# Kernel tuning notes

Hardware: AMD Instinct MI355X
Metric: run time of the kernel (lower is better)

Reference implementation:

```python
import jax, jax.numpy as jnp
import numpy as np

NUM_GROUPS = 32
EPS = 1e-6


def group_norm(x, gamma, beta):
    b, c, h, w = x.shape
    xg = x.reshape(b, NUM_GROUPS, c // NUM_GROUPS, h, w)
    mean = xg.mean(axis=(2, 3, 4), keepdims=True)
    var = xg.var(axis=(2, 3, 4), keepdims=True)
    xn = ((xg - mean) * jax.lax.rsqrt(var + EPS)).reshape(b, c, h, w)
    return xn * gamma[None, :, None, None] + beta[None, :, None, None]


def conv1x1(x, W, b):
    # x: [b,c,h,w], W: [c_out, c_in]
    return jnp.einsum('oi,bihw->bohw', W, x) + b[None, :, None, None]


def setup_inputs() -> dict:
    key = jax.random.key(0)
    ks = jax.random.split(key, 6)
    B, C, H, W = 4, 256, 64, 64
    s = 1.0 / np.sqrt(C)
    return {
        'x': jax.random.normal(ks[0], (B, C, H, W), jnp.float32),
        'gamma': jnp.ones((C,), jnp.float32),
        'beta': jnp.zeros((C,), jnp.float32),
        'Wq': jax.random.normal(ks[1], (C, C), jnp.float32) * s,
        'bq': jnp.zeros((C,), jnp.float32),
        'Wk': jax.random.normal(ks[2], (C, C), jnp.float32) * s,
        'bk': jnp.zeros((C,), jnp.float32),
        'Wv': jax.random.normal(ks[3], (C, C), jnp.float32) * s,
        'bv': jnp.zeros((C,), jnp.float32),
        'Wo': jax.random.normal(ks[4], (C, C), jnp.float32) * s,
        'bo': jnp.zeros((C,), jnp.float32),
    }


def reference(x, gamma, beta, Wq, bq, Wk, bk, Wv, bv, Wo, bo):
    attn_num = 1
    b, c, h, w = x.shape
    hn = group_norm(x, gamma, beta)
    q = conv1x1(hn, Wq, bq)
    k = conv1x1(hn, Wk, bk)
    v = conv1x1(hn, Wv, bv)
    ch = c // attn_num
    n = h * w
    q = q.reshape(b * attn_num, ch, n)
    k = k.reshape(b * attn_num, ch, n)
    v = v.reshape(b * attn_num, ch, n)
    # scores[g, i, j] = sum_c q[g,c,i] * k[g,c,j]; NOTE: scaled by full c, as in source
    scores = jnp.einsum('gci,gcj->gij', q, k) * (float(c) ** -0.5)
    attn = jax.nn.softmax(scores, axis=2)
    # h_[g,c,i] = sum_j v[g,c,j] * attn[g,i,j]
    out = jnp.einsum('gcj,gij->gci', v, attn).reshape(b, c, h, w)
    out = conv1x1(out, Wo, bo)
    return x + out
```

## Files before the change

### kernel.cpp

```cpp
#include <hip/hip_runtime.h>

typedef __attribute__((ext_vector_type(4))) float f32x4;
typedef __attribute__((ext_vector_type(8))) __bf16 bf16x8;

__device__ __forceinline__ unsigned short f2bf(float f) {
  unsigned int u = __float_as_uint(f);
  u += 0x7FFFu + ((u >> 16) & 1u);
  return (unsigned short)(u >> 16);
}
__device__ __forceinline__ float bf2f(unsigned short u) {
  return __uint_as_float(((unsigned int)u) << 16);
}
__device__ __forceinline__ float ex2(float x) {
  return __builtin_amdgcn_exp2f(x);
}

__device__ __forceinline__ void gload16(const void* g, void* l) {
  __builtin_amdgcn_global_load_lds(
      (const __attribute__((address_space(1))) void*)g,
      (__attribute__((address_space(3))) void*)l, 16, 0, 0);
}

#define QSCALE 0.09016844005555897f

__global__ __launch_bounds__(256)
void prep_weights(const float* __restrict__ wq, const float* __restrict__ wk,
                  const float* __restrict__ wv, const float* __restrict__ wo,
                  unsigned short* __restrict__ out) {
  int i = blockIdx.x * 256 + threadIdx.x;
  const float* src = (i < 65536) ? wq : (i < 131072) ? wk : (i < 196608) ? wv : wo;
  out[i] = f2bf(src[i & 65535]);
}

__global__ __launch_bounds__(1024)
void groupnorm_kernel(const float* __restrict__ x, const float* __restrict__ gamma,
                      const float* __restrict__ beta, unsigned short* __restrict__ hnT) {
  const int blk = blockIdx.x;
  const int b = blk >> 5, g = blk & 31;
  const int N = 4096;
  const float* xb = x + ((size_t)b * 256 + (size_t)g * 8) * N;
  const int tid = threadIdx.x;

  float s = 0.f, ss = 0.f;
  for (int c = 0; c < 8; ++c) {
    const float* xc = xb + (size_t)c * N;
    for (int i = tid; i < N; i += 1024) { float v = xc[i]; s += v; ss += v * v; }
  }
  __shared__ float rs[16], rss[16];
  for (int m = 1; m <= 32; m <<= 1) { s += __shfl_xor(s, m); ss += __shfl_xor(ss, m); }
  const int lane = tid & 63, wid = tid >> 6;
  if (lane == 0) { rs[wid] = s; rss[wid] = ss; }
  __syncthreads();
  s = 0.f; ss = 0.f;
  #pragma unroll
  for (int i = 0; i < 16; ++i) { s += rs[i]; ss += rss[i]; }
  const float mean = s * (1.f / 32768.f);
  const float var  = ss * (1.f / 32768.f) - mean * mean;
  const float rstd = rsqrtf(var + 1e-6f);

  float gk[8], bk2[8];
  #pragma unroll
  for (int c = 0; c < 8; ++c) {
    float ga = gamma[g * 8 + c] * rstd;
    gk[c]  = ga;
    bk2[c] = beta[g * 8 + c] - mean * ga;
  }
  unsigned short* outp = hnT + (size_t)b * 256 * N + g * 8;
  for (int i = tid; i < N; i += 1024) {
    union { unsigned short u[8]; uint4 v; } pk;
    #pragma unroll
    for (int c = 0; c < 8; ++c) pk.u[c] = f2bf(xb[(size_t)c * N + i] * gk[c] + bk2[c]);
    *reinterpret_cast<uint4*>(outp + (size_t)i * 256) = pk.v;
  }
}

__global__ __launch_bounds__(256, 2)
void qkv_fused(const unsigned short* __restrict__ WB,
               const unsigned short* __restrict__ hnT,
               const float* __restrict__ bq, const float* __restrict__ bk,
               const float* __restrict__ bv,
               unsigned short* __restrict__ Qt, unsigned short* __restrict__ Kt,
               unsigned short* __restrict__ Vp) {
  __shared__ alignas(1024) unsigned char lds[32768];
  const int tid = threadIdx.x, lane = tid & 63, w = tid >> 6;
  const int hig = lane >> 4, l15 = lane & 15;
  const int z = blockIdx.y, nt = blockIdx.x;
  const int n0 = nt * 32;
  const size_t zoff = (size_t)z * 1048576;
  const unsigned short* hnB = hnT + zoff + (size_t)n0 * 256;

  #pragma unroll
  for (int p = 0; p < 4; ++p) {
    const int idx = p * 256 + tid;
    const int r = idx >> 5, sl = idx & 31;
    gload16(hnB + (size_t)r * 256 + ((sl ^ (r & 7)) << 3), lds + idx * 16);
  }

  const int qs = (lane & 3) ^ ((lane >> 3) & 3);
  const int ar = tid >> 2, asq = tid & 3;
  auto stageA = [&](int d, int s) {
    const unsigned short* base = WB + (s >> 3) * 32768 + (s & 7) * 32 + qs * 8;
    unsigned char* dst = lds + 16384 + d * 8192;
    gload16(base + (size_t)ar * 256,        dst + ar * 64 + asq * 16);
    gload16(base + (size_t)(ar + 64) * 256, dst + (ar + 64) * 64 + asq * 16);
  };

  const int aslot = hig ^ ((l15 >> 1) & 3);
  f32x4 acc[2][2] = {};

  stageA(0, 0);
  __syncthreads();

  for (int s = 0; s < 48; ++s) {
    const int d = s & 1;
    if (s + 1 < 48) stageA(d ^ 1, s + 1);
    const int kt = s & 7;
    bf16x8 af[2];
    #pragma unroll
    for (int mf = 0; mf < 2; ++mf)
      af[mf] = *reinterpret_cast<const bf16x8*>(
          lds + 16384 + d * 8192 + (w * 32 + mf * 16 + l15) * 64 + aslot * 16);
    #pragma unroll
    for (int nf = 0; nf < 2; ++nf) {
      const int rb = nf * 16 + l15;
      bf16x8 bfr = *reinterpret_cast<const bf16x8*>(
          lds + rb * 512 + (((kt * 4 + hig) ^ (rb & 7)) << 4));
      acc[0][nf] = __builtin_amdgcn_mfma_f32_16x16x32_bf16(af[0], bfr, acc[0][nf], 0, 0, 0);
      acc[1][nf] = __builtin_amdgcn_mfma_f32_16x16x32_bf16(af[1], bfr, acc[1][nf], 0, 0, 0);
    }
    if (kt == 7) {
      const int sel = s >> 3, wsel = sel >> 1, mh = sel & 1;
      #pragma unroll
      for (int mf = 0; mf < 2; ++mf) {
        const int gm0 = mh * 128 + w * 32 + mf * 16 + 4 * hig;
        #pragma unroll
        for (int nf = 0; nf < 2; ++nf) {
          const int n = n0 + nf * 16 + l15;
          if (wsel == 0) {
            ushort4 pk;
            pk.x = f2bf((acc[mf][nf][0] + bq[gm0])     * QSCALE);
            pk.y = f2bf((acc[mf][nf][1] + bq[gm0 + 1]) * QSCALE);
            pk.z = f2bf((acc[mf][nf][2] + bq[gm0 + 2]) * QSCALE);
            pk.w = f2bf((acc[mf][nf][3] + bq[gm0 + 3]) * QSCALE);
            *reinterpret_cast<ushort4*>(Qt + zoff + (size_t)n * 256 + gm0) = pk;
          } else if (wsel == 1) {
            ushort4 pk;
            pk.x = f2bf(acc[mf][nf][0] + bk[gm0]);
            pk.y = f2bf(acc[mf][nf][1] + bk[gm0 + 1]);
            pk.z = f2bf(acc[mf][nf][2] + bk[gm0 + 2]);
            pk.w = f2bf(acc[mf][nf][3] + bk[gm0 + 3]);
            *reinterpret_cast<ushort4*>(Kt + zoff + (size_t)n * 256 + gm0) = pk;
          } else {
            #pragma unroll
            for (int e = 0; e < 4; ++e)
              Vp[zoff + (size_t)(gm0 + e) * 4096 + n] = f2bf(acc[mf][nf][e] + bv[gm0 + e]);
          }
          acc[mf][nf] = f32x4{0.f, 0.f, 0.f, 0.f};
        }
      }
    }
    __syncthreads();
  }
}

__global__ __launch_bounds__(256, 2)
void flash_attn(const unsigned short* __restrict__ Qt,
                const unsigned short* __restrict__ Kt,
                const unsigned short* __restrict__ Vp,
                unsigned short* __restrict__ Opart, float* __restrict__ lpart) {
  __shared__ alignas(1024) unsigned char lds[81920];
  const int tid = threadIdx.x, lane = tid & 63, w = tid >> 6;
  const int hig = lane >> 4, l15 = lane & 15;
  const int bid = blockIdx.x;
  const int xcd = bid & 7, k = bid >> 3;
  const int combo = xcd * 2 + (k >> 5);
  const int jh = combo & 3, z = combo >> 2, qtb = k & 31;
  const size_t zoff = (size_t)z * 1048576;
  const unsigned short* Qz = Qt + zoff;
  const unsigned short* Kz = Kt + zoff;
  const unsigned short* Vz = Vp + zoff;
  const int q0 = qtb * 128 + w * 32;
  const int jb0 = jh * 1024;

  bf16x8 qfr[2][8];
  #pragma unroll
  for (int qf = 0; qf < 2; ++qf)
    #pragma unroll
    for (int ks = 0; ks < 8; ++ks)
      qfr[qf][ks] = *reinterpret_cast<const bf16x8*>(
          Qz + (size_t)(q0 + qf * 16 + l15) * 256 + ks * 32 + hig * 8);

  unsigned char* Pw = lds + 65536 + w * 4096;

  const unsigned short* pK[4];
  const unsigned short* pV[4];
  #pragma unroll
  for (int g = 0; g < 4; ++g) {
    const int jr = w * 8 + g * 2 + (lane >> 5);
    pK[g] = Kz + (size_t)(jb0 + jr) * 256 + (((lane & 31) ^ (jr & 7)) << 3);
    const int rloc = lane >> 3;
    const int sraw = (lane & 7) ^ rloc;
    const int cV = 2 * (w * 32 + g * 8 + rloc) + (sraw >> 2);
    pV[g] = Vz + (size_t)cV * 4096 + jb0 + (sraw & 3) * 8;
  }

  auto stage = [&](int d, int t) {
    unsigned char* Kd = lds + d * 16384 + w * 4096;
    unsigned char* Vd = lds + 32768 + d * 16384 + w * 4096;
    #pragma unroll
    for (int g = 0; g < 4; ++g) gload16(pK[g] + (size_t)t * 8192, Kd + g * 1024);
    #pragma unroll
    for (int g = 0; g < 4; ++g) gload16(pV[g] + (size_t)t * 32, Vd + g * 1024);
  };

  f32x4 o0[16] = {}, o1[16] = {};
  float l0 = 0.f, l1 = 0.f;

  stage(0, 0);
  for (int t = 0; t < 32; ++t) {
    asm volatile("s_waitcnt vmcnt(0)" ::: "memory");
    __builtin_amdgcn_s_barrier();
    __builtin_amdgcn_sched_barrier(0);
    const int cur = t & 1;
    if (t + 1 < 32) stage(cur ^ 1, t + 1);

    const unsigned char* Kb = lds + cur * 16384;
    const unsigned char* Vb = lds + 32768 + cur * 16384;

    f32x4 sA[2][2] = {};
    __builtin_amdgcn_s_setprio(1);
    #pragma unroll
    for (int ks = 0; ks < 8; ++ks) {
      #pragma unroll
      for (int jf = 0; jf < 2; ++jf) {
        const int jl = jf * 16 + l15;
        bf16x8 kf = *reinterpret_cast<const bf16x8*>(
            Kb + jl * 512 + (((4 * ks + hig) ^ (jl & 7)) << 4));
        sA[jf][0] = __builtin_amdgcn_mfma_f32_16x16x32_bf16(kf, qfr[0][ks], sA[jf][0], 0, 0, 0);
        sA[jf][1] = __builtin_amdgcn_mfma_f32_16x16x32_bf16(kf, qfr[1][ks], sA[jf][1], 0, 0, 0);
      }
    }
    __builtin_amdgcn_s_setprio(0);

    #pragma unroll
    for (int jf = 0; jf < 2; ++jf) {
      const int so = (((2 * jf + (hig >> 1)) ^ (l15 & 7)) << 4) + ((hig & 1) << 3);
      {
        float p0 = ex2(sA[jf][0][0]), p1 = ex2(sA[jf][0][1]);
        float p2 = ex2(sA[jf][0][2]), p3 = ex2(sA[jf][0][3]);
        l0 += (p0 + p1) + (p2 + p3);
        union { __bf16 b[4]; uint2 u; } pk;
        pk.b[0] = (__bf16)p0; pk.b[1] = (__bf16)p1;
        pk.b[2] = (__bf16)p2; pk.b[3] = (__bf16)p3;
        *reinterpret_cast<uint2*>(Pw + l15 * 128 + so) = pk.u;
      }
      {
        float p0 = ex2(sA[jf][1][0]), p1 = ex2(sA[jf][1][1]);
        float p2 = ex2(sA[jf][1][2]), p3 = ex2(sA[jf][1][3]);
        l1 += (p0 + p1) + (p2 + p3);
        union { __bf16 b[4]; uint2 u; } pk;
        pk.b[0] = (__bf16)p0; pk.b[1] = (__bf16)p1;
        pk.b[2] = (__bf16)p2; pk.b[3] = (__bf16)p3;
        *reinterpret_cast<uint2*>(Pw + (16 + l15) * 128 + so) = pk.u;
      }
    }

    const int pso = (hig ^ (l15 & 7)) << 4;
    bf16x8 pa0 = *reinterpret_cast<const bf16x8*>(Pw + l15 * 128 + pso);
    bf16x8 pa1 = *reinterpret_cast<const bf16x8*>(Pw + (16 + l15) * 128 + pso);
    const int vslot = ((l15 & 1) * 4 + hig) ^ (l15 >> 1);
    __builtin_amdgcn_s_setprio(1);
    #pragma unroll
    for (int nf = 0; nf < 16; ++nf) {
      bf16x8 vb = *reinterpret_cast<const bf16x8*>(
          Vb + (8 * nf + (l15 >> 1)) * 128 + (vslot << 4));
      o0[nf] = __builtin_amdgcn_mfma_f32_16x16x32_bf16(pa0, vb, o0[nf], 0, 0, 0);
      o1[nf] = __builtin_amdgcn_mfma_f32_16x16x32_bf16(pa1, vb, o1[nf], 0, 0, 0);
    }
    __builtin_amdgcn_s_setprio(0);
  }

  l0 += __shfl_xor(l0, 16); l0 += __shfl_xor(l0, 32);
  l1 += __shfl_xor(l1, 16); l1 += __shfl_xor(l1, 32);

  unsigned short* Ob = Opart + ((size_t)(jh * 4 + z) * 4096 + q0) * 256;
  #pragma unroll
  for (int qf = 0; qf < 2; ++qf)
    #pragma unroll
    for (int nf = 0; nf < 16; ++nf)
      #pragma unroll
      for (int e = 0; e < 4; ++e) {
        const int row = qf * 16 + 4 * hig + e;
        Ob[(size_t)row * 256 + nf * 16 + l15] = f2bf((qf == 0) ? o0[nf][e] : o1[nf][e]);
      }
  if (hig == 0) {
    const size_t mb = (size_t)(jh * 4 + z) * 4096 + q0;
    lpart[mb + l15] = l0;  lpart[mb + 16 + l15] = l1;
  }
}

__global__ __launch_bounds__(256)
void flash_merge(const unsigned short* __restrict__ Opart,
                 const float* __restrict__ lpart, unsigned short* __restrict__ Ht) {
  const int t = threadIdx.x;
  const int r = blockIdx.x * 4 + (t >> 6);
  const int c = (t & 63) * 4;
  const int z = r >> 12, n = r & 4095;
  float lsum = 0.f;
  #pragma unroll
  for (int h = 0; h < 4; ++h) lsum += lpart[(h * 4 + z) * 4096 + n];
  const float inv = 1.f / lsum;
  float acc[4] = {};
  #pragma unroll
  for (int h = 0; h < 4; ++h) {
    ushort4 v = *reinterpret_cast<const ushort4*>(
        Opart + ((size_t)((h * 4 + z) * 4096 + n)) * 256 + c);
    acc[0] += bf2f(v.x); acc[1] += bf2f(v.y);
    acc[2] += bf2f(v.z); acc[3] += bf2f(v.w);
  }
  ushort4 pk;
  pk.x = f2bf(acc[0] * inv); pk.y = f2bf(acc[1] * inv);
  pk.z = f2bf(acc[2] * inv); pk.w = f2bf(acc[3] * inv);
  *reinterpret_cast<ushort4*>(Ht + (size_t)r * 256 + c) = pk;
}

__global__ __launch_bounds__(256)
void gemm_out(const unsigned short* __restrict__ A,
              const unsigned short* __restrict__ B, long bStrideZ,
              float* __restrict__ Out, long oStrideZ,
              const float* __restrict__ bias,
              const float* __restrict__ resid, long rStrideZ,
              int M, int N, int K) {
  __shared__ alignas(1024) unsigned char lds[32768];
  const int tid  = threadIdx.x;
  const int lane = tid & 63;
  const int hi   = lane >> 4;
  const int l15  = lane & 15;
  const int wid  = tid >> 6;
  const int wm = wid >> 1, wn = wid & 1;
  const int z  = blockIdx.z;
  const int m0 = blockIdx.y * 128;
  const int n0 = blockIdx.x * 128;
  const unsigned short* Az = A;
  const unsigned short* Bz = B + (size_t)z * bStrideZ;

  const int c0 = wid * 2, c1 = wid * 2 + 1;
  const int rr = lane >> 2;
  const int qs = (lane & 3) ^ ((lane >> 3) & 3);
  const unsigned short* pa0 = Az + (size_t)(m0 + c0 * 16 + rr) * K + qs * 8;
  const unsigned short* pa1 = Az + (size_t)(m0 + c1 * 16 + rr) * K + qs * 8;
  const unsigned short* pb0 = Bz + (size_t)(n0 + c0 * 16 + rr) * K + qs * 8;
  const unsigned short* pb1 = Bz + (size_t)(n0 + c1 * 16 + rr) * K + qs * 8;
  unsigned char* lA0 = lds + c0 * 1024;
  unsigned char* lA1 = lds + c1 * 1024;
  unsigned char* lB0 = lds + 8192 + c0 * 1024;
  unsigned char* lB1 = lds + 8192 + c1 * 1024;

  const int slot = hi ^ ((l15 >> 1) & 3);
  int roffA[4], roffB[4];
  #pragma unroll
  for (int t = 0; t < 4; ++t) {
    roffA[t] = (wm * 64 + t * 16 + l15) * 64 + slot * 16;
    roffB[t] = 8192 + (wn * 64 + t * 16 + l15) * 64 + slot * 16;
  }

  f32x4 acc[4][4] = {};

  const int nk = K >> 5;
  gload16(pa0, lA0); gload16(pa1, lA1);
  gload16(pb0, lB0); gload16(pb1, lB1);
  __syncthreads();

  int cur = 0;
  for (int kt = 0; kt < nk; ++kt) {
    if (kt + 1 < nk) {
      const size_t ko = (size_t)(kt + 1) * 32;
      const int bo = (cur ^ 1) * 16384;
      gload16(pa0 + ko, lA0 + bo); gload16(pa1 + ko, lA1 + bo);
      gload16(pb0 + ko, lB0 + bo); gload16(pb1 + ko, lB1 + bo);
    }
    const unsigned char* base = lds + cur * 16384;
    bf16x8 af[4], bfr[4];
    #pragma unroll
    for (int t = 0; t < 4; ++t) {
      af[t]  = *reinterpret_cast<const bf16x8*>(base + roffA[t]);
      bfr[t] = *reinterpret_cast<const bf16x8*>(base + roffB[t]);
    }
    #pragma unroll
    for (int mt = 0; mt < 4; ++mt)
      #pragma unroll
      for (int nt = 0; nt < 4; ++nt)
        acc[mt][nt] = __builtin_amdgcn_mfma_f32_16x16x32_bf16(af[mt], bfr[nt], acc[mt][nt], 0, 0, 0);
    __syncthreads();
    cur ^= 1;
  }

  const int gmb = m0 + wm * 64;
  const int gnb = n0 + wn * 64;
  float* O = Out + (size_t)z * oStrideZ;
  const float* R = resid + (size_t)z * rStrideZ;
  #pragma unroll
  for (int mt = 0; mt < 4; ++mt) {
    const int gm0 = gmb + mt * 16 + 4 * hi;
    #pragma unroll
    for (int nt = 0; nt < 4; ++nt) {
      const int gn = gnb + nt * 16 + l15;
      #pragma unroll
      for (int e = 0; e < 4; ++e) {
        size_t idx = (size_t)(gm0 + e) * N + gn;
        O[idx] = acc[mt][nt][e] + bias[gm0 + e] + R[idx];
      }
    }
  }
}

__global__ void ws_too_small(float* out, float v) {
  if (threadIdx.x == 0 && blockIdx.x == 0) out[0] = v;
}

extern "C" void kernel_launch(void* const* d_in, const int* in_sizes, int n_in,
                              void* d_out, int out_size, void* d_ws, size_t ws_size,
                              hipStream_t stream) {
  const float* x     = (const float*)d_in[0];
  const float* gamma = (const float*)d_in[1];
  const float* beta  = (const float*)d_in[2];
  const float* Wq    = (const float*)d_in[3];
  const float* bq    = (const float*)d_in[4];
  const float* Wk    = (const float*)d_in[5];
  const float* bk    = (const float*)d_in[6];
  const float* Wv    = (const float*)d_in[7];
  const float* bv    = (const float*)d_in[8];
  const float* Wo    = (const float*)d_in[9];
  const float* bo    = (const float*)d_in[10];
  float* out = (float*)d_out;

  unsigned char* ws = (unsigned char*)d_ws;
  unsigned short* WB    = (unsigned short*)(ws);
  unsigned short* hnT   = (unsigned short*)(ws + 524288);
  float*          lpart = (float*)(ws + 524288);
  unsigned short* Qt    = (unsigned short*)(ws + 8912896);
  unsigned short* Kt    = (unsigned short*)(ws + 17301504);
  unsigned short* V     = (unsigned short*)(ws + 25690112);
  unsigned short* Ht    = (unsigned short*)(ws + 34078720);
  unsigned short* Opart = (unsigned short*)(ws + 42467328);

  if (ws_size < 76283904) {
    hipMemsetAsync(d_out, 0, (size_t)out_size * 4, stream);
    ws_too_small<<<1, 64, 0, stream>>>(out, (float)ws_size);
    return;
  }

  prep_weights<<<1024, 256, 0, stream>>>(Wq, Wk, Wv, Wo, WB);
  groupnorm_kernel<<<128, 1024, 0, stream>>>(x, gamma, beta, hnT);

  qkv_fused<<<dim3(128, 4), 256, 0, stream>>>(WB, hnT, bq, bk, bv, Qt, Kt, V);

  flash_attn<<<512, 256, 0, stream>>>(Qt, Kt, V, Opart, lpart);
  flash_merge<<<4096, 256, 0, stream>>>(Opart, lpart, Ht);

  gemm_out<<<dim3(32, 2, 4), 256, 0, stream>>>(
      WB + 196608, Ht, 1048576, out, 1048576, bo, x, 1048576, 256, 4096, 256);
}
```

Baseline: 145.3 us.

## Split groupnorm across twice as many blocks using cooperative grid sync

Replaces the 128-block groupnorm with a 256-block cooperative kernel. Each block handles half of a (batch, group) slice, keeps its values in registers, writes partial sums, synchronizes the whole grid, then normalizes and writes the bf16 transposed output. The aim is to use more of the GPU's CUs for this memory-bound step and avoid re-reading x. In exchange it depends on cooperative launch and pays for a grid-wide barrier, and it falls back to the old kernel if the launch fails.

```diff
diff --git a/kernel.cpp b/kernel.cpp
--- a/kernel.cpp
+++ b/kernel.cpp
@@ -1,4 +1,7 @@
 #include <hip/hip_runtime.h>
+#include <hip/hip_cooperative_groups.h>
+
+namespace cg = cooperative_groups;
 
 typedef __attribute__((ext_vector_type(4))) float f32x4;
 typedef __attribute__((ext_vector_type(8))) __bf16 bf16x8;
@@ -30,6 +33,61 @@
   int i = blockIdx.x * 256 + threadIdx.x;
   const float* src = (i < 65536) ? wq : (i < 131072) ? wk : (i < 196608) ? wv : wo;
   out[i] = f2bf(src[i & 65535]);
+}
+
+__global__ __launch_bounds__(512)
+void groupnorm_coop(const float* __restrict__ x, const float* __restrict__ gamma,
+                    const float* __restrict__ beta, unsigned short* __restrict__ hnT,
+                    float2* __restrict__ part) {
+  const int blk = blockIdx.x;
+  const int h = blk & 1, bg = blk >> 1;
+  const int b = bg >> 5, g = bg & 31;
+  const int tid = threadIdx.x;
+  const float* xb = x + ((size_t)b * 256 + (size_t)g * 8) * 4096 + h * 2048;
+
+  float v[8][4];
+  float s = 0.f, ss = 0.f;
+  #pragma unroll
+  for (int c = 0; c < 8; ++c)
+    #pragma unroll
+    for (int s2 = 0; s2 < 4; ++s2) {
+      float val = xb[c * 4096 + s2 * 512 + tid];
+      v[c][s2] = val; s += val; ss += val * val;
+    }
+  __shared__ float rs[8], rss[8];
+  for (int m = 1; m <= 32; m <<= 1) { s += __shfl_xor(s, m); ss += __shfl_xor(ss, m); }
+  const int lane = tid & 63, wid = tid >> 6;
+  if (lane == 0) { rs[wid] = s; rss[wid] = ss; }
+  __syncthreads();
+  if (tid == 0) {
+    float a = 0.f, b2 = 0.f;
+    #pragma unroll
+    for (int i = 0; i < 8; ++i) { a += rs[i]; b2 += rss[i]; }
+    part[blk] = make_float2(a, b2);
+  }
+  cg::this_grid().sync();
+  const int base = blk & ~1;
+  const float2 p0 = part[base], p1 = part[base + 1];
+  const float mean = (p0.x + p1.x) * (1.f / 32768.f);
+  const float var  = (p0.y + p1.y) * (1.f / 32768.f) - mean * mean;
+  const float rstd = rsqrtf(var + 1e-6f);
+
+  float gk[8], bk2[8];
+  #pragma unroll
+  for (int c = 0; c < 8; ++c) {
+    float ga = gamma[g * 8 + c] * rstd;
+    gk[c]  = ga;
+    bk2[c] = beta[g * 8 + c] - mean * ga;
+  }
+  unsigned short* outp = hnT + (size_t)b * 4096 * 256 + g * 8;
+  #pragma unroll
+  for (int s2 = 0; s2 < 4; ++s2) {
+    const int n = h * 2048 + s2 * 512 + tid;
+    union { unsigned short u[8]; uint4 q; } pk;
+    #pragma unroll
+    for (int c = 0; c < 8; ++c) pk.u[c] = f2bf(v[c][s2] * gk[c] + bk2[c]);
+    *reinterpret_cast<uint4*>(outp + (size_t)n * 256) = pk.q;
+  }
 }
 
 __global__ __launch_bounds__(1024)
@@ -443,6 +501,7 @@
   unsigned short* V     = (unsigned short*)(ws + 25690112);
   unsigned short* Ht    = (unsigned short*)(ws + 34078720);
   unsigned short* Opart = (unsigned short*)(ws + 42467328);
+  float2*         gnpart = (float2*)(ws + 76021760);
 
   if (ws_size < 76283904) {
     hipMemsetAsync(d_out, 0, (size_t)out_size * 4, stream);
@@ -451,7 +510,15 @@
   }
 
   prep_weights<<<1024, 256, 0, stream>>>(Wq, Wk, Wv, Wo, WB);
-  groupnorm_kernel<<<128, 1024, 0, stream>>>(x, gamma, beta, hnT);
+
+  {
+    void* gnargs[] = {(void*)&x, (void*)&gamma, (void*)&beta, (void*)&hnT, (void*)&gnpart};
+    hipError_t ce = hipLaunchCooperativeKernel((const void*)groupnorm_coop,
+                                               dim3(256), dim3(512), gnargs, 0, stream);
+    if (ce != hipSuccess) {
+      groupnorm_kernel<<<128, 1024, 0, stream>>>(x, gamma, beta, hnT);
+    }
+  }
 
   qkv_fused<<<dim3(128, 4), 256, 0, stream>>>(WB, hnT, bq, bk, bv, Qt, Kt, V);
 
```

Result: slower. 169.9 us (+17.0%).

## Split group-norm across two blocks per group and keep inputs in registers

Applied to the files above, without the earlier changes.

The group-norm kernel now launches 256 blocks of 512 threads, so each group is handled by two blocks, and the grid covers more compute units than the old 128-block launch. Each block keeps its half of the group in registers and reuses those values for the normalized output instead of reading x a second time. To get full-group statistics, each block still reads the other half, so total reads stay roughly the same but are spread over twice as many blocks. Holding 32 values per thread raises register pressure.

```diff
diff --git a/kernel.cpp b/kernel.cpp
--- a/kernel.cpp
+++ b/kernel.cpp
@@ -32,28 +32,41 @@
   out[i] = f2bf(src[i & 65535]);
 }
 
-__global__ __launch_bounds__(1024)
-void groupnorm_kernel(const float* __restrict__ x, const float* __restrict__ gamma,
-                      const float* __restrict__ beta, unsigned short* __restrict__ hnT) {
+__global__ __launch_bounds__(512)
+void groupnorm_split(const float* __restrict__ x, const float* __restrict__ gamma,
+                     const float* __restrict__ beta, unsigned short* __restrict__ hnT) {
   const int blk = blockIdx.x;
-  const int b = blk >> 5, g = blk & 31;
-  const int N = 4096;
-  const float* xb = x + ((size_t)b * 256 + (size_t)g * 8) * N;
+  const int h = blk & 1, bg = blk >> 1;
+  const int b = bg >> 5, g = bg & 31;
   const int tid = threadIdx.x;
-
+  const float* xg = x + ((size_t)b * 256 + (size_t)g * 8) * 4096;
+  const float* xo = xg + h * 2048;
+  const float* xr = xg + (h ^ 1) * 2048;
+
+  float v[8][4];
   float s = 0.f, ss = 0.f;
-  for (int c = 0; c < 8; ++c) {
-    const float* xc = xb + (size_t)c * N;
-    for (int i = tid; i < N; i += 1024) { float v = xc[i]; s += v; ss += v * v; }
-  }
-  __shared__ float rs[16], rss[16];
+  #pragma unroll
+  for (int c = 0; c < 8; ++c)
+    #pragma unroll
+    for (int s2 = 0; s2 < 4; ++s2) {
+      float val = xo[c * 4096 + s2 * 512 + tid];
+      v[c][s2] = val; s += val; ss += val * val;
+    }
+  #pragma unroll
+  for (int c = 0; c < 8; ++c)
+    #pragma unroll
+    for (int s2 = 0; s2 < 4; ++s2) {
+      float val = xr[c * 4096 + s2 * 512 + tid];
+      s += val; ss += val * val;
+    }
+  __shared__ float rs[8], rss[8];
   for (int m = 1; m <= 32; m <<= 1) { s += __shfl_xor(s, m); ss += __shfl_xor(ss, m); }
   const int lane = tid & 63, wid = tid >> 6;
   if (lane == 0) { rs[wid] = s; rss[wid] = ss; }
   __syncthreads();
   s = 0.f; ss = 0.f;
   #pragma unroll
-  for (int i = 0; i < 16; ++i) { s += rs[i]; ss += rss[i]; }
+  for (int i = 0; i < 8; ++i) { s += rs[i]; ss += rss[i]; }
   const float mean = s * (1.f / 32768.f);
   const float var  = ss * (1.f / 32768.f) - mean * mean;
   const float rstd = rsqrtf(var + 1e-6f);
@@ -65,12 +78,14 @@
     gk[c]  = ga;
     bk2[c] = beta[g * 8 + c] - mean * ga;
   }
-  unsigned short* outp = hnT + (size_t)b * 256 * N + g * 8;
-  for (int i = tid; i < N; i += 1024) {
-    union { unsigned short u[8]; uint4 v; } pk;
-    #pragma unroll
-    for (int c = 0; c < 8; ++c) pk.u[c] = f2bf(xb[(size_t)c * N + i] * gk[c] + bk2[c]);
-    *reinterpret_cast<uint4*>(outp + (size_t)i * 256) = pk.v;
+  unsigned short* outp = hnT + (size_t)b * 4096 * 256 + g * 8;
+  #pragma unroll
+  for (int s2 = 0; s2 < 4; ++s2) {
+    const int n = h * 2048 + s2 * 512 + tid;
+    union { unsigned short u[8]; uint4 q; } pk;
+    #pragma unroll
+    for (int c = 0; c < 8; ++c) pk.u[c] = f2bf(v[c][s2] * gk[c] + bk2[c]);
+    *reinterpret_cast<uint4*>(outp + (size_t)n * 256) = pk.q;
   }
 }
 
@@ -451,7 +466,7 @@
   }
 
   prep_weights<<<1024, 256, 0, stream>>>(Wq, Wk, Wv, Wo, WB);
-  groupnorm_kernel<<<128, 1024, 0, stream>>>(x, gamma, beta, hnT);
+  groupnorm_split<<<256, 512, 0, stream>>>(x, gamma, beta, hnT);
 
   qkv_fused<<<dim3(128, 4), 256, 0, stream>>>(WB, hnT, bq, bk, bv, Qt, Kt, V);
 
```

Result: faster. 137.1 us (-5.7%).
